# Kernel tuning notes

Hardware: AMD Instinct MI355X
Metric: run time of the kernel (lower is better)

Reference implementation:

```python
import jax, jax.numpy as jnp
import numpy as np


def setup_inputs() -> dict:
    key = jax.random.key(0)
    kq, kk, kv, ki, ks = jax.random.split(key, 5)
    B, H, S, D, VD, T = 2, 8, 2048, 64, 64, 128
    q = jax.random.normal(kq, (B, H, S, D), dtype=jnp.float32)
    k = jax.random.normal(kk, (B, H, S, D), dtype=jnp.float32)
    v = jax.random.normal(kv, (B, H, S, VD), dtype=jnp.float32)
    topk_indices = jax.random.randint(ki, (B, S, T), 0, S, dtype=jnp.int64)
    topk_scores = jax.random.uniform(ks, (B, S, T), dtype=jnp.float32)
    return {"q": q, "k": k, "v": v, "topk_indices": topk_indices,
            "topk_scores": topk_scores}


def reference(q, k, v, topk_indices, topk_scores):
    # q: (B,H,S,D), k: (B,H,S,D), v: (B,H,S,VD), topk_indices: (B,S,T)
    head_dim = q.shape[-1]
    scale = head_dim ** (-0.5)

    # Gather selected K/V per query directly (no O(S^2) expansion).
    # For each batch b: kb (H,S,D), idx (S,T) -> kb[:, idx, :] (H,S,T,D)
    gather = jax.vmap(lambda xb, ib: xb[:, ib, :])
    k_g = gather(k, topk_indices)  # (B,H,S,T,D)
    v_g = gather(v, topk_indices)  # (B,H,S,T,VD)

    # (B,H,S,T) scores
    attn_scores = jnp.einsum('bhsd,bhstd->bhst', q, k_g) * scale
    attn_weights = jax.nn.softmax(attn_scores, axis=-1)

    # reweight by indexer scores (broadcast over heads), then renormalize
    attn_weights = attn_weights * topk_scores[:, None, :, :]
    attn_weights = attn_weights / (attn_weights.sum(axis=-1, keepdims=True) + 1e-12)

    # (B,H,S,VD)
    output = jnp.einsum('bhst,bhstd->bhsd', attn_weights, v_g)
    return output
```

## Files before the change

kernel.cpp:

```cpp
#include <hip/hip_runtime.h>
#include <math.h>


#define BB 2
#define HH 8
#define SS 2048
#define DD 64
#define VDD 64
#define TT 128
#define SCALE 0.125f
#define NKV (BB * HH * SS * DD)

__device__ __forceinline__ float bf_lo(unsigned int u) {
    return __uint_as_float(u << 16);
}
__device__ __forceinline__ float bf_hi(unsigned int u) {
    return __uint_as_float(u & 0xFFFF0000u);
}
__device__ __forceinline__ unsigned short f2bf_rne(float f) {
    unsigned int u = __float_as_uint(f);
    u += 0x7FFFu + ((u >> 16) & 1u);
    return (unsigned short)(u >> 16);
}

__global__ __launch_bounds__(256) void cvt_kv_bf16(
    const float* __restrict__ k, const float* __restrict__ v,
    unsigned int* __restrict__ kb, unsigned int* __restrict__ vb)
{
    int i = (blockIdx.x * 256 + threadIdx.x) * 4;
    if (i >= NKV) return;
    float4 kf = *(const float4*)(k + i);
    float4 vf = *(const float4*)(v + i);
    unsigned int k0 = (unsigned int)f2bf_rne(kf.x) | ((unsigned int)f2bf_rne(kf.y) << 16);
    unsigned int k1 = (unsigned int)f2bf_rne(kf.z) | ((unsigned int)f2bf_rne(kf.w) << 16);
    unsigned int v0 = (unsigned int)f2bf_rne(vf.x) | ((unsigned int)f2bf_rne(vf.y) << 16);
    unsigned int v1 = (unsigned int)f2bf_rne(vf.z) | ((unsigned int)f2bf_rne(vf.w) << 16);
    *(uint2*)(kb + i / 2) = make_uint2(k0, k1);
    *(uint2*)(vb + i / 2) = make_uint2(v0, v1);
}

__global__ __launch_bounds__(256, 4) void dsa_sparse_attn_bf16(
    const float* __restrict__ q,
    const unsigned int* __restrict__ kb,
    const unsigned int* __restrict__ vb,
    const int* __restrict__ topk_idx,
    const float* __restrict__ topk_sc,
    float* __restrict__ out)
{
    const int tid  = threadIdx.x;
    const int wave = tid >> 6;
    const int lane = tid & 63;

    const int plane = blockIdx.x & 15;
    const int s4    = blockIdx.x >> 4;
    const int s     = s4 * 4 + wave;
    const int b     = plane >> 3;

    const float*        qp  = q  + ((size_t)plane * SS + s) * DD;
    const unsigned int* kp  = kb + (size_t)plane * SS * (DD / 2);
    const unsigned int* vp  = vb + (size_t)plane * SS * (VDD / 2);
    const int*          ip  = topk_idx + ((size_t)b * SS + s) * TT;
    const float*        scp = topk_sc  + ((size_t)b * SS + s) * TT;
    float*              op  = out + ((size_t)plane * SS + s) * VDD;

    __shared__ int   s_idx[4][TT];
    __shared__ float s_w[4][TT];

    int   i0  = ip[lane];
    int   i1  = ip[64 + lane];
    float sc0 = scp[lane];
    float sc1 = scp[64 + lane];
    s_idx[wave][lane]      = i0;
    s_idx[wave][64 + lane] = i1;

    const int h = lane & 7;
    const int g = lane >> 3;
    float qf[8];
    {
        float4 qa = *(const float4*)(qp + h * 8);
        float4 qb = *(const float4*)(qp + h * 8 + 4);
        qf[0] = qa.x; qf[1] = qa.y; qf[2] = qa.z; qf[3] = qa.w;
        qf[4] = qb.x; qf[5] = qb.y; qf[6] = qb.z; qf[7] = qb.w;
    }

    __syncthreads();

    #pragma unroll
    for (int tc = 0; tc < 16; ++tc) {
        int t   = tc * 8 + g;
        int idx = s_idx[wave][t];
        uint4 kk = *(const uint4*)(kp + (size_t)idx * 32 + h * 4);
        float acc;
        acc  = qf[0] * bf_lo(kk.x) + qf[1] * bf_hi(kk.x);
        acc += qf[2] * bf_lo(kk.y) + qf[3] * bf_hi(kk.y);
        acc += qf[4] * bf_lo(kk.z) + qf[5] * bf_hi(kk.z);
        acc += qf[6] * bf_lo(kk.w) + qf[7] * bf_hi(kk.w);
        acc += __shfl_xor(acc, 1);
        acc += __shfl_xor(acc, 2);
        acc += __shfl_xor(acc, 4);
        if (h == 0) s_w[wave][t] = acc * SCALE;
    }
    __syncthreads();

    float a0 = s_w[wave][lane];
    float a1 = s_w[wave][64 + lane];
    float m = fmaxf(a0, a1);
    #pragma unroll
    for (int off = 32; off >= 1; off >>= 1)
        m = fmaxf(m, __shfl_xor(m, off));
    float e0 = __expf(a0 - m) * sc0;
    float e1 = __expf(a1 - m) * sc1;
    float sum = e0 + e1;
    #pragma unroll
    for (int off = 32; off >= 1; off >>= 1)
        sum += __shfl_xor(sum, off);
    float inv = 1.0f / (sum + 1e-12f);
    s_w[wave][lane]      = e0 * inv;
    s_w[wave][64 + lane] = e1 * inv;
    __syncthreads();

    const int half = lane >> 5;
    const int li   = lane & 31;
    float ax = 0.f, ay = 0.f;
    #pragma unroll 8
    for (int tc = 0; tc < 64; ++tc) {
        int   t   = tc * 2 + half;
        int   idx = s_idx[wave][t];
        float w   = s_w[wave][t];
        unsigned int u = vp[(size_t)idx * 32 + li];
        ax = fmaf(w, bf_lo(u), ax);
        ay = fmaf(w, bf_hi(u), ay);
    }
    ax += __shfl_xor(ax, 32);
    ay += __shfl_xor(ay, 32);
    if (half == 0)
        *(float2*)(op + li * 2) = make_float2(ax, ay);
}

__global__ __launch_bounds__(256, 4) void dsa_sparse_attn_f32(
    const float* __restrict__ q,
    const float* __restrict__ k,
    const float* __restrict__ v,
    const int* __restrict__ topk_idx,
    const float* __restrict__ topk_sc,
    float* __restrict__ out)
{
    const int tid  = threadIdx.x;
    const int wave = tid >> 6;
    const int lane = tid & 63;
    const int plane = blockIdx.x & 15;
    const int s     = (blockIdx.x >> 4) * 4 + wave;
    const int b     = plane >> 3;

    const float* qp  = q + ((size_t)plane * SS + s) * DD;
    const float* kp  = k + (size_t)plane * SS * DD;
    const float* vp  = v + (size_t)plane * SS * VDD;
    const int*   ip  = topk_idx + ((size_t)b * SS + s) * TT;
    const float* scp = topk_sc  + ((size_t)b * SS + s) * TT;
    float*       op  = out + ((size_t)plane * SS + s) * VDD;

    __shared__ int   s_idx[4][TT];
    __shared__ float s_w[4][TT];

    float sc0 = scp[lane];
    float sc1 = scp[64 + lane];
    s_idx[wave][lane]      = ip[lane];
    s_idx[wave][64 + lane] = ip[64 + lane];

    const int l = lane & 3;
    const int g = lane >> 2;
    float4 qf[4];
    #pragma unroll
    for (int j = 0; j < 4; ++j) qf[j] = *(const float4*)(qp + l * 4 + 16 * j);
    __syncthreads();

    #pragma unroll
    for (int tc = 0; tc < 8; ++tc) {
        int t = tc * 16 + g;
        const float* krow = kp + (size_t)s_idx[wave][t] * DD;
        float acc = 0.f;
        #pragma unroll
        for (int j = 0; j < 4; ++j) {
            float4 kf = *(const float4*)(krow + l * 4 + 16 * j);
            acc += qf[j].x * kf.x + qf[j].y * kf.y + qf[j].z * kf.z + qf[j].w * kf.w;
        }
        acc += __shfl_xor(acc, 1);
        acc += __shfl_xor(acc, 2);
        if (l == 0) s_w[wave][t] = acc * SCALE;
    }
    __syncthreads();

    float a0 = s_w[wave][lane];
    float a1 = s_w[wave][64 + lane];
    float m = fmaxf(a0, a1);
    #pragma unroll
    for (int off = 32; off >= 1; off >>= 1) m = fmaxf(m, __shfl_xor(m, off));
    float e0 = __expf(a0 - m) * sc0;
    float e1 = __expf(a1 - m) * sc1;
    float sum = e0 + e1;
    #pragma unroll
    for (int off = 32; off >= 1; off >>= 1) sum += __shfl_xor(sum, off);
    float inv = 1.0f / (sum + 1e-12f);
    s_w[wave][lane]      = e0 * inv;
    s_w[wave][64 + lane] = e1 * inv;
    __syncthreads();

    float acc = 0.f;
    #pragma unroll 8
    for (int t = 0; t < TT; ++t)
        acc = fmaf(s_w[wave][t], vp[(size_t)s_idx[wave][t] * VDD + lane], acc);
    op[lane] = acc;
}

extern "C" void kernel_launch(void* const* d_in, const int* in_sizes, int n_in,
                              void* d_out, int out_size, void* d_ws, size_t ws_size,
                              hipStream_t stream) {
    const float* q   = (const float*)d_in[0];
    const float* k   = (const float*)d_in[1];
    const float* v   = (const float*)d_in[2];
    const int*   idx = (const int*)d_in[3];
    const float* sc  = (const float*)d_in[4];
    float*       out = (float*)d_out;

    const size_t need = (size_t)NKV * 2 * 2;
    if (ws_size >= need) {
        unsigned int* kb = (unsigned int*)d_ws;
        unsigned int* vb = kb + NKV / 2;
        hipLaunchKernelGGL(cvt_kv_bf16, dim3(NKV / 4 / 256), dim3(256), 0, stream,
                           k, v, kb, vb);
        hipLaunchKernelGGL(dsa_sparse_attn_bf16, dim3(8192), dim3(256), 0, stream,
                           q, kb, vb, idx, sc, out);
    } else {
        hipLaunchKernelGGL(dsa_sparse_attn_f32, dim3(8192), dim3(256), 0, stream,
                           q, k, v, idx, sc, out);
    }
}
```

Before: 134.0 us.

## Use 16-byte V gathers, pack weight/index in LDS, skip bf16 high mask

The V accumulation loop now has each lane load a 16-byte chunk of a gathered V row, covering eight rows per wave per step, where it used to load four bytes per lane. Partial sums are then combined with cross-lane shuffles before the store. Softmax weights and indices are packed into one uint2 LDS array, so a single read yields both. The bf16 high-half mask is dropped, which leaves the low 16 bits as mantissa noise in the high value: a small precision error traded for fewer ALU operations.

```diff
diff --git a/kernel.cpp b/kernel.cpp
--- a/kernel.cpp
+++ b/kernel.cpp
@@ -15,7 +15,7 @@
     return __uint_as_float(u << 16);
 }
 __device__ __forceinline__ float bf_hi(unsigned int u) {
-    return __uint_as_float(u & 0xFFFF0000u);
+    return __uint_as_float(u);
 }
 __device__ __forceinline__ unsigned short f2bf_rne(float f) {
     unsigned int u = __float_as_uint(f);
@@ -50,10 +50,11 @@
     const int tid  = threadIdx.x;
     const int wave = tid >> 6;
     const int lane = tid & 63;
+    const int h    = lane & 7;
+    const int g    = lane >> 3;
 
     const int plane = blockIdx.x & 15;
-    const int s4    = blockIdx.x >> 4;
-    const int s     = s4 * 4 + wave;
+    const int s     = (blockIdx.x >> 4) * 4 + wave;
     const int b     = plane >> 3;
 
     const float*        qp  = q  + ((size_t)plane * SS + s) * DD;
@@ -63,47 +64,37 @@
     const float*        scp = topk_sc  + ((size_t)b * SS + s) * TT;
     float*              op  = out + ((size_t)plane * SS + s) * VDD;
 
-    __shared__ int   s_idx[4][TT];
-    __shared__ float s_w[4][TT];
-
-    int   i0  = ip[lane];
-    int   i1  = ip[64 + lane];
+    __shared__ uint2 s_wi[4][TT];
+
     float sc0 = scp[lane];
     float sc1 = scp[64 + lane];
-    s_idx[wave][lane]      = i0;
-    s_idx[wave][64 + lane] = i1;
-
-    const int h = lane & 7;
-    const int g = lane >> 3;
-    float qf[8];
-    {
-        float4 qa = *(const float4*)(qp + h * 8);
-        float4 qb = *(const float4*)(qp + h * 8 + 4);
-        qf[0] = qa.x; qf[1] = qa.y; qf[2] = qa.z; qf[3] = qa.w;
-        qf[4] = qb.x; qf[5] = qb.y; qf[6] = qb.z; qf[7] = qb.w;
-    }
+    s_wi[wave][lane].y      = (unsigned int)ip[lane];
+    s_wi[wave][64 + lane].y = (unsigned int)ip[64 + lane];
+
+    float4 qa = *(const float4*)(qp + h * 8);
+    float4 qb = *(const float4*)(qp + h * 8 + 4);
 
     __syncthreads();
 
     #pragma unroll
     for (int tc = 0; tc < 16; ++tc) {
         int t   = tc * 8 + g;
-        int idx = s_idx[wave][t];
+        int idx = (int)s_wi[wave][t].y;
         uint4 kk = *(const uint4*)(kp + (size_t)idx * 32 + h * 4);
         float acc;
-        acc  = qf[0] * bf_lo(kk.x) + qf[1] * bf_hi(kk.x);
-        acc += qf[2] * bf_lo(kk.y) + qf[3] * bf_hi(kk.y);
-        acc += qf[4] * bf_lo(kk.z) + qf[5] * bf_hi(kk.z);
-        acc += qf[6] * bf_lo(kk.w) + qf[7] * bf_hi(kk.w);
+        acc  = qa.x * bf_lo(kk.x) + qa.y * bf_hi(kk.x);
+        acc += qa.z * bf_lo(kk.y) + qa.w * bf_hi(kk.y);
+        acc += qb.x * bf_lo(kk.z) + qb.y * bf_hi(kk.z);
+        acc += qb.z * bf_lo(kk.w) + qb.w * bf_hi(kk.w);
         acc += __shfl_xor(acc, 1);
         acc += __shfl_xor(acc, 2);
         acc += __shfl_xor(acc, 4);
-        if (h == 0) s_w[wave][t] = acc * SCALE;
-    }
-    __syncthreads();
-
-    float a0 = s_w[wave][lane];
-    float a1 = s_w[wave][64 + lane];
+        if (h == 0) s_wi[wave][t].x = __float_as_uint(acc * SCALE);
+    }
+    __syncthreads();
+
+    float a0 = __uint_as_float(s_wi[wave][lane].x);
+    float a1 = __uint_as_float(s_wi[wave][64 + lane].x);
     float m = fmaxf(a0, a1);
     #pragma unroll
     for (int off = 32; off >= 1; off >>= 1)
@@ -115,26 +106,32 @@
     for (int off = 32; off >= 1; off >>= 1)
         sum += __shfl_xor(sum, off);
     float inv = 1.0f / (sum + 1e-12f);
-    s_w[wave][lane]      = e0 * inv;
-    s_w[wave][64 + lane] = e1 * inv;
-    __syncthreads();
-
-    const int half = lane >> 5;
-    const int li   = lane & 31;
-    float ax = 0.f, ay = 0.f;
-    #pragma unroll 8
-    for (int tc = 0; tc < 64; ++tc) {
-        int   t   = tc * 2 + half;
-        int   idx = s_idx[wave][t];
-        float w   = s_w[wave][t];
-        unsigned int u = vp[(size_t)idx * 32 + li];
-        ax = fmaf(w, bf_lo(u), ax);
-        ay = fmaf(w, bf_hi(u), ay);
-    }
-    ax += __shfl_xor(ax, 32);
-    ay += __shfl_xor(ay, 32);
-    if (half == 0)
-        *(float2*)(op + li * 2) = make_float2(ax, ay);
+    s_wi[wave][lane].x      = __float_as_uint(e0 * inv);
+    s_wi[wave][64 + lane].x = __float_as_uint(e1 * inv);
+    __syncthreads();
+
+    float a[8] = {0.f, 0.f, 0.f, 0.f, 0.f, 0.f, 0.f, 0.f};
+    #pragma unroll
+    for (int i = 0; i < 16; ++i) {
+        uint2 wi = s_wi[wave][i * 8 + g];
+        float w  = __uint_as_float(wi.x);
+        int  idx = (int)wi.y;
+        uint4 u = *(const uint4*)(vp + (size_t)idx * 32 + h * 4);
+        a[0] = fmaf(w, bf_lo(u.x), a[0]);  a[1] = fmaf(w, bf_hi(u.x), a[1]);
+        a[2] = fmaf(w, bf_lo(u.y), a[2]);  a[3] = fmaf(w, bf_hi(u.y), a[3]);
+        a[4] = fmaf(w, bf_lo(u.z), a[4]);  a[5] = fmaf(w, bf_hi(u.z), a[5]);
+        a[6] = fmaf(w, bf_lo(u.w), a[6]);  a[7] = fmaf(w, bf_hi(u.w), a[7]);
+    }
+    #pragma unroll
+    for (int j = 0; j < 8; ++j) {
+        a[j] += __shfl_xor(a[j], 8);
+        a[j] += __shfl_xor(a[j], 16);
+        a[j] += __shfl_xor(a[j], 32);
+    }
+    if (g == 0) {
+        *(float4*)(op + h * 8)     = make_float4(a[0], a[1], a[2], a[3]);
+        *(float4*)(op + h * 8 + 4) = make_float4(a[4], a[5], a[6], a[7]);
+    }
 }
 
 __global__ __launch_bounds__(256, 4) void dsa_sparse_attn_f32(
```

Measured after the change: 130.7 us. 1.03x faster.
